# Performance work log

Hardware: AMD Instinct MI355X
Metric: run time of the kernel (lower is better)

The kernel has to match this reference:

```python
import jax, jax.numpy as jnp
import numpy as np

HIDDEN_DIM = 128

def setup_inputs() -> dict:
    key = jax.random.key(0)
    kq, kk, kv = jax.random.split(key, 3)
    B, S, D = 32, 2048, HIDDEN_DIM
    q = jax.random.normal(kq, (B, S, D), dtype=jnp.float32)
    k = jax.random.normal(kk, (B, S, D), dtype=jnp.float32)
    v = jax.random.normal(kv, (B, S, D), dtype=jnp.float32)
    return {"q": q, "k": k, "v": v}

def reference(q, k, v):
    # scores: [B, Sq, Sk]
    scale = jnp.asarray(np.sqrt(1.0 / HIDDEN_DIM), dtype=q.dtype)
    scores = jnp.einsum('bqd,bkd->bqk', q, k) * scale
    attention = jax.nn.softmax(scores, axis=2)  # dropout p=0.0 -> identity
    context = jnp.einsum('bqk,bkd->bqd', attention, v)
    return (context, attention)
```

## Files before the change

kernel.cpp:

```cpp
#include <hip/hip_runtime.h>

typedef _Float16 half8 __attribute__((ext_vector_type(8)));
typedef _Float16 half4 __attribute__((ext_vector_type(4)));
typedef float    f32x4v __attribute__((ext_vector_type(4)));

constexpr int S    = 2048;
constexpr int D    = 128;
constexpr int TQ   = 32;
constexpr int QB   = S / TQ;
constexpr int CPW  = 256;
constexpr int NT   = CPW / 16;
constexpr int PPAD = 8;
constexpr float SCALE = 0.08838834764831845f;

__launch_bounds__(1024, 4)
__global__ void attn_fwd(const float* __restrict__ Q,
                         const float* __restrict__ K,
                         const float* __restrict__ V,
                         float* __restrict__ Oc,
                         float* __restrict__ Oa)
{
    const int nper = gridDim.x >> 3;
    const int bid  = blockIdx.x;
    const int swz  = (bid & 7) * nper + (bid >> 3);
    const int b    = swz / QB;
    const int q0   = (swz % QB) * TQ;

    const int tid  = threadIdx.x;
    const int wave = tid >> 6;
    const int wr   = wave >> 3;
    const int wc   = wave & 7;
    const int lane = tid & 63;
    const int l15  = lane & 15;
    const int g    = lane >> 4;

    __shared__ _Float16 Pbuf[2][TQ][CPW + PPAD];
    __shared__ float red[16][16];
    __shared__ float gmax[TQ];
    __shared__ float grs[TQ];

    const float* qrow = Q + ((size_t)b * S + (q0 + wr * 16 + l15)) * D;
    half8 qf[4];
#pragma unroll
    for (int ks = 0; ks < 4; ++ks) {
        const int d0 = ks * 32 + g * 8;
        f32x4v a = *(const f32x4v*)(qrow + d0);
        f32x4v c = *(const f32x4v*)(qrow + d0 + 4);
        half8 h;
        h[0]=(_Float16)a[0]; h[1]=(_Float16)a[1]; h[2]=(_Float16)a[2]; h[3]=(_Float16)a[3];
        h[4]=(_Float16)c[0]; h[5]=(_Float16)c[1]; h[6]=(_Float16)c[2]; h[7]=(_Float16)c[3];
        qf[ks] = h;
    }

    const float* kbase = K + (size_t)b * S * D;
    f32x4v acc[NT];
#pragma unroll
    for (int t = 0; t < NT; ++t) { acc[t][0]=0.f; acc[t][1]=0.f; acc[t][2]=0.f; acc[t][3]=0.f; }
#pragma unroll
    for (int t = 0; t < NT; ++t) {
        const float* krow = kbase + (size_t)(wc * CPW + t * 16 + l15) * D;
#pragma unroll
        for (int ks = 0; ks < 4; ++ks) {
            const int d0 = ks * 32 + g * 8;
            f32x4v x = *(const f32x4v*)(krow + d0);
            f32x4v y = *(const f32x4v*)(krow + d0 + 4);
            half8 kf;
            kf[0]=(_Float16)x[0]; kf[1]=(_Float16)x[1]; kf[2]=(_Float16)x[2]; kf[3]=(_Float16)x[3];
            kf[4]=(_Float16)y[0]; kf[5]=(_Float16)y[1]; kf[6]=(_Float16)y[2]; kf[7]=(_Float16)y[3];
            acc[t] = __builtin_amdgcn_mfma_f32_16x16x32_f16(qf[ks], kf, acc[t], 0, 0, 0);
        }
    }

    float mx[4];
#pragma unroll
    for (int r = 0; r < 4; ++r) {
        float m = -1e30f;
#pragma unroll
        for (int t = 0; t < NT; ++t) {
            acc[t][r] *= SCALE;
            m = fmaxf(m, acc[t][r]);
        }
#pragma unroll
        for (int off = 1; off < 16; off <<= 1)
            m = fmaxf(m, __shfl_xor(m, off, 64));
        mx[r] = m;
    }
    if (l15 == 0) {
#pragma unroll
        for (int r = 0; r < 4; ++r) red[wave][g * 4 + r] = mx[r];
    }
    __syncthreads();
    if (tid < TQ) {
        const int wr_ = tid >> 4, lr = tid & 15;
        float m = red[wr_ * 8][lr];
#pragma unroll
        for (int w = 1; w < 8; ++w) m = fmaxf(m, red[wr_ * 8 + w][lr]);
        gmax[tid] = m;
    }
    __syncthreads();

    float sm[4];
#pragma unroll
    for (int r = 0; r < 4; ++r) {
        const float gm = gmax[wr * 16 + g * 4 + r];
        float s = 0.0f;
#pragma unroll
        for (int t = 0; t < NT; ++t) {
            float p = __expf(acc[t][r] - gm);
            acc[t][r] = p;
            s += p;
        }
#pragma unroll
        for (int off = 1; off < 16; off <<= 1)
            s += __shfl_xor(s, off, 64);
        sm[r] = s;
    }
    if (l15 == 0) {
#pragma unroll
        for (int r = 0; r < 4; ++r) red[wave][g * 4 + r] = sm[r];
    }
    __syncthreads();
    if (tid < TQ) {
        const int wr_ = tid >> 4, lr = tid & 15;
        float s = 0.0f;
#pragma unroll
        for (int w = 0; w < 8; ++w) s += red[wr_ * 8 + w][lr];
        grs[tid] = 1.0f / s;
    }
    __syncthreads();

    float rv[4];
#pragma unroll
    for (int r = 0; r < 4; ++r) rv[r] = grs[wr * 16 + g * 4 + r];

    float* oab = Oa + ((size_t)b * S + q0 + wr * 16) * S + wc * CPW;
    half4 ph[NT];
#pragma unroll
    for (int t = 0; t < NT; ++t) {
        const int c = t * 16 + l15;
#pragma unroll
        for (int r = 0; r < 4; ++r) {
            float pn = acc[t][r] * rv[r];
            ph[t][r] = (_Float16)pn;
            oab[(size_t)(g * 4 + r) * S + c] = pn;
        }
    }

    auto write_slice = [&](int bi) {
#pragma unroll
        for (int t = 0; t < NT; ++t) {
            const int c = t * 16 + l15;
#pragma unroll
            for (int r = 0; r < 4; ++r)
                Pbuf[bi][wr * 16 + g * 4 + r][c] = ph[t][r];
        }
    };

    const float* vb0 = V + (size_t)b * S * D + (wc * 16 + l15);
    f32x4v ctx; ctx[0]=0.f; ctx[1]=0.f; ctx[2]=0.f; ctx[3]=0.f;

    if (wc == 0) write_slice(0);
    __syncthreads();

    for (int cw = 0; cw < 8; ++cw) {
        if (wc == cw + 1) write_slice((cw + 1) & 1);
        const _Float16* prow = &Pbuf[cw & 1][wr * 16 + l15][g * 8];
        const float* vb = vb0 + (size_t)(cw * CPW + g * 8) * D;
#pragma unroll
        for (int mf = 0; mf < 8; ++mf) {
            half8 pf = *(const half8*)(prow + mf * 32);
            half8 vf;
#pragma unroll
            for (int j = 0; j < 8; ++j)
                vf[j] = (_Float16)vb[(size_t)(mf * 32 + j) * D];
            ctx = __builtin_amdgcn_mfma_f32_16x16x32_f16(pf, vf, ctx, 0, 0, 0);
        }
        __syncthreads();
    }

    float* ocb = Oc + ((size_t)b * S + q0 + wr * 16) * D + (wc * 16 + l15);
#pragma unroll
    for (int r = 0; r < 4; ++r)
        ocb[(size_t)(g * 4 + r) * D] = ctx[r];
}

extern "C" void kernel_launch(void* const* d_in, const int* in_sizes, int n_in,
                              void* d_out, int out_size, void* d_ws, size_t ws_size,
                              hipStream_t stream) {
    const float* q = (const float*)d_in[0];
    const float* k = (const float*)d_in[1];
    const float* v = (const float*)d_in[2];
    const int B = in_sizes[0] / (S * D);
    float* ctx  = (float*)d_out;
    float* attn = ctx + (size_t)B * S * D;
    dim3 grid(B * QB);
    attn_fwd<<<grid, dim3(1024), 0, stream>>>(q, k, v, ctx, attn);
}
```

Measured before the change: 1.325 ms.

## Stage V through swizzled LDS with register prefetch and transpose QK MFMA output

Swaps the MFMA operand order so each lane holds four consecutive key columns of one query row. This allows the attention matrix to be written with 16-byte vector stores instead of scalar strided stores, and simplifies the row reductions. V is now loaded cooperatively into a double-buffered, XOR-swizzled LDS tile of 64 keys, prefetched two chunks ahead through registers, replacing per-wave strided scalar global gathers. The cost is more loop iterations and barriers (32 chunks instead of 8) and added LDS usage.

```diff
diff --git a/kernel.cpp b/kernel.cpp
--- a/kernel.cpp
+++ b/kernel.cpp
@@ -4,13 +4,14 @@
 typedef _Float16 half4 __attribute__((ext_vector_type(4)));
 typedef float    f32x4v __attribute__((ext_vector_type(4)));
 
-constexpr int S    = 2048;
-constexpr int D    = 128;
-constexpr int TQ   = 32;
-constexpr int QB   = S / TQ;
-constexpr int CPW  = 256;
-constexpr int NT   = CPW / 16;
-constexpr int PPAD = 8;
+constexpr int S   = 2048;
+constexpr int D   = 128;
+constexpr int TQ  = 32;
+constexpr int QB  = S / TQ;
+constexpr int CPW = 256;
+constexpr int NT  = CPW / 16;
+constexpr int CK  = 64;
+constexpr int NC  = S / CK;
 constexpr float SCALE = 0.08838834764831845f;
 
 __launch_bounds__(1024, 4)
@@ -34,21 +35,22 @@
     const int l15  = lane & 15;
     const int g    = lane >> 4;
 
-    __shared__ _Float16 Pbuf[2][TQ][CPW + PPAD];
+    __shared__ _Float16 Vlds[2][128][64];
+    __shared__ _Float16 Pbuf[2][TQ][64];
     __shared__ float red[16][16];
     __shared__ float gmax[TQ];
     __shared__ float grs[TQ];
 
-    const float* qrow = Q + ((size_t)b * S + (q0 + wr * 16 + l15)) * D;
+    const float* qrow_p = Q + ((size_t)b * S + (q0 + wr * 16 + l15)) * D;
     half8 qf[4];
 #pragma unroll
     for (int ks = 0; ks < 4; ++ks) {
         const int d0 = ks * 32 + g * 8;
-        f32x4v a = *(const f32x4v*)(qrow + d0);
-        f32x4v c = *(const f32x4v*)(qrow + d0 + 4);
+        f32x4v x = *(const f32x4v*)(qrow_p + d0);
+        f32x4v y = *(const f32x4v*)(qrow_p + d0 + 4);
         half8 h;
-        h[0]=(_Float16)a[0]; h[1]=(_Float16)a[1]; h[2]=(_Float16)a[2]; h[3]=(_Float16)a[3];
-        h[4]=(_Float16)c[0]; h[5]=(_Float16)c[1]; h[6]=(_Float16)c[2]; h[7]=(_Float16)c[3];
+        h[0]=(_Float16)x[0]; h[1]=(_Float16)x[1]; h[2]=(_Float16)x[2]; h[3]=(_Float16)x[3];
+        h[4]=(_Float16)y[0]; h[5]=(_Float16)y[1]; h[6]=(_Float16)y[2]; h[7]=(_Float16)y[3];
         qf[ks] = h;
     }
 
@@ -67,112 +69,118 @@
             half8 kf;
             kf[0]=(_Float16)x[0]; kf[1]=(_Float16)x[1]; kf[2]=(_Float16)x[2]; kf[3]=(_Float16)x[3];
             kf[4]=(_Float16)y[0]; kf[5]=(_Float16)y[1]; kf[6]=(_Float16)y[2]; kf[7]=(_Float16)y[3];
-            acc[t] = __builtin_amdgcn_mfma_f32_16x16x32_f16(qf[ks], kf, acc[t], 0, 0, 0);
-        }
-    }
-
-    float mx[4];
-#pragma unroll
-    for (int r = 0; r < 4; ++r) {
-        float m = -1e30f;
-#pragma unroll
-        for (int t = 0; t < NT; ++t) {
-            acc[t][r] *= SCALE;
-            m = fmaxf(m, acc[t][r]);
-        }
-#pragma unroll
-        for (int off = 1; off < 16; off <<= 1)
-            m = fmaxf(m, __shfl_xor(m, off, 64));
-        mx[r] = m;
-    }
-    if (l15 == 0) {
-#pragma unroll
-        for (int r = 0; r < 4; ++r) red[wave][g * 4 + r] = mx[r];
-    }
+            acc[t] = __builtin_amdgcn_mfma_f32_16x16x32_f16(kf, qf[ks], acc[t], 0, 0, 0);
+        }
+    }
+
+    float m = -1e30f;
+#pragma unroll
+    for (int t = 0; t < NT; ++t) {
+        acc[t] *= SCALE;
+#pragma unroll
+        for (int r = 0; r < 4; ++r) m = fmaxf(m, acc[t][r]);
+    }
+    m = fmaxf(m, __shfl_xor(m, 16, 64));
+    m = fmaxf(m, __shfl_xor(m, 32, 64));
+    if (lane < 16) red[wave][l15] = m;
     __syncthreads();
     if (tid < TQ) {
         const int wr_ = tid >> 4, lr = tid & 15;
-        float m = red[wr_ * 8][lr];
-#pragma unroll
-        for (int w = 1; w < 8; ++w) m = fmaxf(m, red[wr_ * 8 + w][lr]);
-        gmax[tid] = m;
-    }
-    __syncthreads();
-
-    float sm[4];
-#pragma unroll
-    for (int r = 0; r < 4; ++r) {
-        const float gm = gmax[wr * 16 + g * 4 + r];
-        float s = 0.0f;
-#pragma unroll
-        for (int t = 0; t < NT; ++t) {
+        float mm = red[wr_ * 8][lr];
+#pragma unroll
+        for (int w = 1; w < 8; ++w) mm = fmaxf(mm, red[wr_ * 8 + w][lr]);
+        gmax[tid] = mm;
+    }
+    __syncthreads();
+
+    const float gm = gmax[wr * 16 + l15];
+    float sum = 0.0f;
+#pragma unroll
+    for (int t = 0; t < NT; ++t) {
+#pragma unroll
+        for (int r = 0; r < 4; ++r) {
             float p = __expf(acc[t][r] - gm);
             acc[t][r] = p;
-            s += p;
-        }
-#pragma unroll
-        for (int off = 1; off < 16; off <<= 1)
-            s += __shfl_xor(s, off, 64);
-        sm[r] = s;
-    }
-    if (l15 == 0) {
-#pragma unroll
-        for (int r = 0; r < 4; ++r) red[wave][g * 4 + r] = sm[r];
-    }
+            sum += p;
+        }
+    }
+    sum += __shfl_xor(sum, 16, 64);
+    sum += __shfl_xor(sum, 32, 64);
+    if (lane < 16) red[wave][l15] = sum;
     __syncthreads();
     if (tid < TQ) {
         const int wr_ = tid >> 4, lr = tid & 15;
-        float s = 0.0f;
-#pragma unroll
-        for (int w = 0; w < 8; ++w) s += red[wr_ * 8 + w][lr];
-        grs[tid] = 1.0f / s;
-    }
-    __syncthreads();
-
-    float rv[4];
-#pragma unroll
-    for (int r = 0; r < 4; ++r) rv[r] = grs[wr * 16 + g * 4 + r];
-
-    float* oab = Oa + ((size_t)b * S + q0 + wr * 16) * S + wc * CPW;
+        float ss = 0.0f;
+#pragma unroll
+        for (int w = 0; w < 8; ++w) ss += red[wr_ * 8 + w][lr];
+        grs[tid] = 1.0f / ss;
+    }
+    __syncthreads();
+
+    const float rv = grs[wr * 16 + l15];
+    float* oar = Oa + ((size_t)b * S + q0 + wr * 16 + l15) * S + wc * CPW + g * 4;
     half4 ph[NT];
 #pragma unroll
     for (int t = 0; t < NT; ++t) {
-        const int c = t * 16 + l15;
-#pragma unroll
-        for (int r = 0; r < 4; ++r) {
-            float pn = acc[t][r] * rv[r];
-            ph[t][r] = (_Float16)pn;
-            oab[(size_t)(g * 4 + r) * S + c] = pn;
-        }
-    }
-
-    auto write_slice = [&](int bi) {
-#pragma unroll
-        for (int t = 0; t < NT; ++t) {
-            const int c = t * 16 + l15;
-#pragma unroll
-            for (int r = 0; r < 4; ++r)
-                Pbuf[bi][wr * 16 + g * 4 + r][c] = ph[t][r];
-        }
+        f32x4v pn = acc[t] * rv;
+        *(f32x4v*)(oar + t * 16) = pn;
+        half4 h; h[0]=(_Float16)pn[0]; h[1]=(_Float16)pn[1]; h[2]=(_Float16)pn[2]; h[3]=(_Float16)pn[3];
+        ph[t] = h;
+    }
+
+    const int sd  = tid & 127;
+    const int skq = tid >> 7;
+    const float* vsrc = V + (size_t)b * S * D + sd;
+
+    float vr[2][8];
+    f32x4v ctx; ctx[0]=0.f; ctx[1]=0.f; ctx[2]=0.f; ctx[3]=0.f;
+    const int prow = wr * 16 + l15;
+    const int vrow = wc * 16 + l15;
+
+    auto stage_load = [&](float* dst, int cc) {
+#pragma unroll
+        for (int i = 0; i < 8; ++i)
+            dst[i] = vsrc[(size_t)(cc * CK + skq * 8 + i) * D];
     };
-
-    const float* vb0 = V + (size_t)b * S * D + (wc * 16 + l15);
-    f32x4v ctx; ctx[0]=0.f; ctx[1]=0.f; ctx[2]=0.f; ctx[3]=0.f;
-
-    if (wc == 0) write_slice(0);
-    __syncthreads();
-
-    for (int cw = 0; cw < 8; ++cw) {
-        if (wc == cw + 1) write_slice((cw + 1) & 1);
-        const _Float16* prow = &Pbuf[cw & 1][wr * 16 + l15][g * 8];
-        const float* vb = vb0 + (size_t)(cw * CPW + g * 8) * D;
-#pragma unroll
-        for (int mf = 0; mf < 8; ++mf) {
-            half8 pf = *(const half8*)(prow + mf * 32);
-            half8 vf;
-#pragma unroll
-            for (int j = 0; j < 8; ++j)
-                vf[j] = (_Float16)vb[(size_t)(mf * 32 + j) * D];
+    auto stage_write = [&](int cc, const float* src) {
+        half8 vh;
+#pragma unroll
+        for (int i = 0; i < 8; ++i) vh[i] = (_Float16)src[i];
+        *(half8*)&Vlds[cc & 1][sd][(skq ^ (sd & 7)) << 3] = vh;
+    };
+
+    stage_load(vr[0], 0);
+    stage_write(0, vr[0]);
+    if (wc == 0) {
+#pragma unroll
+        for (int tt = 0; tt < 4; ++tt) {
+            const int gi = tt * 2 + (g >> 1);
+            *(half4*)&Pbuf[0][prow][((gi ^ (prow & 7)) << 3) + ((g & 1) << 2)] = ph[tt];
+        }
+    }
+    stage_load(vr[1], 1);
+    __syncthreads();
+
+#pragma unroll
+    for (int c = 0; c < NC; ++c) {
+        if (c + 1 < NC) {
+            stage_write(c + 1, vr[(c + 1) & 1]);
+            if (wc == ((c + 1) >> 2)) {
+                const int sub = (c + 1) & 3;
+#pragma unroll
+                for (int tt = 0; tt < 4; ++tt) {
+                    const int gi = tt * 2 + (g >> 1);
+                    *(half4*)&Pbuf[(c + 1) & 1][prow][((gi ^ (prow & 7)) << 3) + ((g & 1) << 2)]
+                        = ph[sub * 4 + tt];
+                }
+            }
+        }
+        if (c + 2 < NC) stage_load(vr[c & 1], c + 2);
+#pragma unroll
+        for (int mf = 0; mf < 2; ++mf) {
+            const int gi = mf * 4 + g;
+            half8 pf = *(const half8*)&Pbuf[c & 1][prow][((gi ^ (prow & 7)) << 3)];
+            half8 vf = *(const half8*)&Vlds[c & 1][vrow][((gi ^ (vrow & 7)) << 3)];
             ctx = __builtin_amdgcn_mfma_f32_16x16x32_f16(pf, vf, ctx, 0, 0, 0);
         }
         __syncthreads();
```

Measured after the change: 1.256 ms. -5.2%, faster.
